# Kernel tuning notes

Hardware: AMD Instinct MI355X
Metric: run time of the kernel (lower is better)

## Reference

```python
import jax, jax.numpy as jnp
import numpy as np

B, T, L = 8, 5, 16          # meta-batch, inner (train) steps, test examples per task
C, H, W = 3, 64, 64
NCLS = 100
FEAT = 256 * (H // 16) * (W // 16)  # 4096
CHANS = [(C, 32), (32, 64), (64, 128), (128, 256), (256, 256)]
DN = ('NCHW', 'OIHW', 'NCHW')


def setup_inputs() -> dict:
    key = jax.random.key(0)
    ks = jax.random.split(key, 16)
    inp = {}
    for j, (ic, oc) in enumerate(CHANS):
        std = 1.0 / np.sqrt(ic * 9)
        inp[f"w{j}"] = jax.random.normal(ks[j], (oc, ic, 3, 3), jnp.float32) * std
        inp[f"b{j}"] = jnp.zeros((oc,), jnp.float32)
    inp["W_out"] = jax.random.normal(ks[5], (NCLS, FEAT), jnp.float32) / np.sqrt(FEAT)
    inp["b_out"] = jnp.zeros((NCLS,), jnp.float32)
    inp["inner_log_lr"] = jnp.asarray(np.log(0.01), jnp.float32)
    inp["train_x"] = jax.random.normal(ks[6], (B, T, C, H, W), jnp.float32)
    inp["test_x"] = jax.random.normal(ks[7], (B, L, C, H, W), jnp.float32)
    inp["train_gate"] = jax.random.uniform(ks[8], (B, T, FEAT), dtype=jnp.float32)
    inp["test_gate"] = jax.random.uniform(ks[9], (B, L, FEAT), dtype=jnp.float32)
    inp["train_y"] = jax.random.randint(ks[10], (B, T), 0, NCLS)
    inp["test_y"] = jax.random.randint(ks[11], (B, L), 0, NCLS)
    inp["evaluate"] = 1
    return inp


def _conv(x, w, b, s):
    # x: [N, C, H, W]; per-example weight w: [OC, IC, 3, 3]; 'same'-ish pad=1
    y = jax.lax.conv_general_dilated(x, w, (s, s), [(1, 1), (1, 1)], dimension_numbers=DN)
    return jax.nn.relu(y + b[None, :, None, None])


def _features(fw, x, gate):
    # x: [B, L, C, H, W]; fw: tuple of per-example (batched) params
    for j in range(5):
        s = 1 if j == 0 else 2
        x = jax.vmap(_conv, in_axes=(0, 0, 0, None))(x, fw[2 * j], fw[2 * j + 1], s)
    return x.reshape(x.shape[0], x.shape[1], -1) * gate  # [B, L, FEAT]


def _ce(logits, y):
    return -jnp.take_along_axis(jax.nn.log_softmax(logits, -1), y[..., None], -1)[..., 0]


def _forward(params, log_lr, train_x, test_x, train_gate, test_gate, train_y, test_y):
    b = train_x.shape[0]
    lr = jnp.exp(log_lr)
    # per-example fast weights (MAML)
    fw = tuple(jnp.broadcast_to(p, (b,) + p.shape) for p in params)

    def step(fw, batch):
        xi, yi, gi = batch  # [B,C,H,W], [B], [B,FEAT]
        def loss_fn(fw):
            f = _features(fw, xi[:, None], gi[:, None])[:, 0]  # [B, FEAT]
            logit = jnp.einsum('bnm,bm->bn', fw[10], f) + fw[11]
            return _ce(logit, yi).sum()
        g = jax.grad(loss_fn)(fw)
        return tuple(w - lr * gw for w, gw in zip(fw, g)), None

    fw, _ = jax.lax.scan(
        step, fw,
        (jnp.swapaxes(train_x, 0, 1), jnp.swapaxes(train_y, 0, 1), jnp.swapaxes(train_gate, 0, 1)))

    f = _features(fw, test_x, test_gate)                         # [B, L, FEAT]
    logit = jnp.einsum('bnm,blm->bln', fw[10], f) + fw[11][:, None, :]
    loss = _ce(logit, test_y)[..., None]                          # [B, L, 1]
    return loss, lr, logit


def reference(w0, b0, w1, b1, w2, b2, w3, b3, w4, b4, W_out, b_out, inner_log_lr,
              train_x, test_x, train_gate, test_gate, train_y, test_y, evaluate):
    params = (w0, b0, w1, b1, w2, b2, w3, b3, w4, b4, W_out, b_out)
    loss, lr, logit = _forward(params, inner_log_lr, train_x, test_x,
                               train_gate, test_gate, train_y, test_y)
    evaluation = (jnp.argmax(logit, -1) == test_y) if evaluate else None
    return (loss, lr, evaluation, logit)
```

## Files before the change

### kernel.cpp

```cpp
#include <hip/hip_runtime.h>

#define NB 8
#define NT 5
#define NL 16
#define NCLS 100
#define FEAT 4096
#define CHW (3*64*64)

#define OFF_W0 0
#define OFF_B0 864
#define OFF_W1 896
#define OFF_B1 19328
#define OFF_W2 19392
#define OFF_B2 93120
#define OFF_W3 93248
#define OFF_B3 388160
#define OFF_W4 388416
#define OFF_B4 978240
#define OFF_WO 978496
#define OFF_BO 1388096
#define PT     1388196

#define A1 0
#define A2 131072
#define A3 196608
#define A4 229376
#define A5 245760
#define ATOT 249856

struct Params12 { const float* p[12]; };

__global__ void bcast_kernel(Params12 ps, float* __restrict__ fw) {
    const int offs[13] = {OFF_W0,OFF_B0,OFF_W1,OFF_B1,OFF_W2,OFF_B2,OFF_W3,OFF_B3,
                          OFF_W4,OFF_B4,OFF_WO,OFF_BO,PT};
    long idx = (long)blockIdx.x * blockDim.x + threadIdx.x;
    long total = (long)NB * PT;
    if (idx >= total) return;
    int i = (int)(idx % PT);
    int j = 11;
    while (j > 0 && i < offs[j]) --j;
    fw[idx] = ps.p[j][i - offs[j]];
}

template<int IC,int IH,int IW,int OC,int OH,int OW,int S,int UF,int BS>
__global__ __launch_bounds__(BS) void conv_fwd_u(
    const float* __restrict__ xb, long x_ts,
    const float* __restrict__ fw, int woff, int boff,
    float* __restrict__ yb, long y_ts)
{
    constexpr int OHW = OH*OW, IHW = IH*IW;
    long idx = (long)blockIdx.x * BS + threadIdx.x;
    int pix = (int)(idx % OHW); long r = idx / OHW;
    int oc = (int)(r % OC); int b = (int)(r / OC);
    int oh = pix / OW, ow = pix % OW;
    int ih0 = oh*S - 1, iw0 = ow*S - 1;

    const float* x = xb + (long)b * x_ts;
    const float* w = fw + (long)b * PT + woff + (long)oc * IC * 9;
    float acc = fw[(long)b * PT + boff + oc];

    #pragma unroll 1
    for (int ic0 = 0; ic0 < IC; ic0 += UF) {
        float xv[UF][9];
        #pragma unroll
        for (int u = 0; u < UF; ++u) {
            const float* xc = x + (long)(ic0 + u) * IHW;
            #pragma unroll
            for (int kh = 0; kh < 3; ++kh) {
                int ih = ih0 + kh;
                #pragma unroll
                for (int kw = 0; kw < 3; ++kw) {
                    int iw = iw0 + kw;
                    bool v = ((unsigned)ih < (unsigned)IH) && ((unsigned)iw < (unsigned)IW);
                    xv[u][kh*3+kw] = v ? xc[ih*IW + iw] : 0.f;
                }
            }
        }
        #pragma unroll
        for (int u = 0; u < UF; ++u) {
            const float* wc = w + (ic0 + u) * 9;
            #pragma unroll
            for (int k = 0; k < 9; ++k)
                acc += xv[u][k] * wc[k];
        }
    }
    yb[(long)b * y_ts + (long)oc * OHW + pix] = fmaxf(acc, 0.f);
}

template<int IC,int IH,int IW,int OC,int OH,int OW,int S,int UF,int BS,int KS>
__global__ __launch_bounds__(BS) void conv_fwd_uks(
    const float* __restrict__ xb, long x_ts,
    const float* __restrict__ fw, int woff,
    float* __restrict__ pb)
{
    constexpr int OHW = OH*OW, IHW = IH*IW;
    constexpr int ICC = IC/KS;
    long idx = (long)blockIdx.x * BS + threadIdx.x;
    int pix = (int)(idx % OHW); long r = idx / OHW;
    int oc = (int)(r % OC); r /= OC;
    int ks = (int)(r % KS); int b = (int)(r / KS);
    int oh = pix / OW, ow = pix % OW;
    int ih0 = oh*S - 1, iw0 = ow*S - 1;

    const float* x = xb + (long)b * x_ts;
    const float* w = fw + (long)b * PT + woff + (long)oc * IC * 9;
    float acc = 0.f;

    #pragma unroll 1
    for (int ic0 = ks*ICC; ic0 < (ks+1)*ICC; ic0 += UF) {
        float xv[UF][9];
        #pragma unroll
        for (int u = 0; u < UF; ++u) {
            const float* xc = x + (long)(ic0 + u) * IHW;
            #pragma unroll
            for (int kh = 0; kh < 3; ++kh) {
                int ih = ih0 + kh;
                #pragma unroll
                for (int kw = 0; kw < 3; ++kw) {
                    int iw = iw0 + kw;
                    bool v = ((unsigned)ih < (unsigned)IH) && ((unsigned)iw < (unsigned)IW);
                    xv[u][kh*3+kw] = v ? xc[ih*IW + iw] : 0.f;
                }
            }
        }
        #pragma unroll
        for (int u = 0; u < UF; ++u) {
            const float* wc = w + (ic0 + u) * 9;
            #pragma unroll
            for (int k = 0; k < 9; ++k)
                acc += xv[u][k] * wc[k];
        }
    }
    pb[((long)ks*NB + b) * ((long)OC*OHW) + (long)oc*OHW + pix] = acc;
}

template<int IC,int IH,int IW,int OC,int OH,int OW,int S,int UF,int KS>
__global__ __launch_bounds__(64) void conv_fwd_us(
    const float* __restrict__ xb, long x_ts,
    const float* __restrict__ fw, int woff,
    float* __restrict__ pb)
{
    constexpr int OHW = OH*OW, IHW = IH*IW, ICC = IC/KS;
    static_assert(OHW == 64, "one wave = one oc-plane");
    int bi = blockIdx.x;
    int oc = bi % OC; int ks = (bi / OC) % KS; int b = bi / (OC*KS);
    int pix = threadIdx.x;
    int oh = pix / OW, ow = pix % OW;
    int ih0 = oh*S - 1, iw0 = ow*S - 1;

    const float* x = xb + (long)b * x_ts;
    const float* w = fw + (long)b * PT + woff + (long)oc * IC * 9;

    float acc = 0.f;
    #pragma unroll 1
    for (int ic0 = ks*ICC; ic0 < (ks+1)*ICC; ic0 += UF) {
        float xv[UF][9];
        #pragma unroll
        for (int u = 0; u < UF; ++u) {
            const float* xc = x + (long)(ic0 + u) * IHW;
            #pragma unroll
            for (int kh = 0; kh < 3; ++kh) {
                int ih = ih0 + kh;
                #pragma unroll
                for (int kw = 0; kw < 3; ++kw) {
                    int iw = iw0 + kw;
                    bool v = ((unsigned)ih < (unsigned)IH) && ((unsigned)iw < (unsigned)IW);
                    xv[u][kh*3+kw] = v ? xc[ih*IW + iw] : 0.f;
                }
            }
        }
        #pragma unroll
        for (int u = 0; u < UF; ++u) {
            const float* wc = w + (ic0 + u) * 9;
            #pragma unroll
            for (int k = 0; k < 9; ++k)
                acc += xv[u][k] * wc[k];
        }
    }
    pb[((long)ks*NB + b) * ((long)OC*OHW) + (long)oc*OHW + pix] = acc;
}

template<int IC,int IH,int IW,int OC,int OH,int OW,int S,int TOC,int NSUB,int ICB>
__global__ __launch_bounds__(256) void conv_fwd2(
    const float* __restrict__ xb, long x_ts, long x_es,
    const float* __restrict__ fw, int woff, int boff,
    float* __restrict__ yb, long y_ts, int N)
{
    constexpr int OHW = OH*OW, IHW = IH*IW;
    constexpr int PPB = 256/NSUB;
    constexpr int TILES = OHW/PPB;
    constexpr int OCB = NSUB*TOC;
    constexpr int NOCG = OC/OCB;
    __shared__ float wlds[ICB*9*OCB];

    int bi = blockIdx.x;
    int tile = bi % TILES;
    int ocg  = (bi / TILES) % NOCG;
    int n    = (bi / (TILES*NOCG)) % N;
    int b    = bi / (TILES*NOCG*N);

    int tid = threadIdx.x;
    int pixl = tid % PPB, sub = tid / PPB;
    int pix = tile * PPB + pixl;
    int oc0 = ocg * OCB + sub * TOC;
    int oh = pix / OW, ow = pix % OW;
    int ih0 = oh*S - 1, iw0 = ow*S - 1;

    const float* xp  = xb + (long)b * x_ts + (long)n * x_es;
    const float* fwp = fw + (long)b * PT + woff;
    const float* bp  = fw + (long)b * PT + boff;

    float acc[TOC];
    #pragma unroll
    for (int t = 0; t < TOC; ++t) acc[t] = bp[oc0 + t];

    #pragma unroll 1
    for (int ic0i = 0; ic0i < IC; ic0i += ICB) {
        __syncthreads();
        for (int i = tid; i < ICB*9*OCB; i += 256) {
            int o = i % OCB; int rem = i / OCB; int k = rem % 9; int icb = rem / 9;
            wlds[i] = fwp[((long)(ocg*OCB + o) * IC + ic0i + icb) * 9 + k];
        }
        __syncthreads();
        #pragma unroll 2
        for (int icb = 0; icb < ICB; ++icb) {
            const float* xc = xp + (long)(ic0i + icb) * IHW;
            float xv[9];
            #pragma unroll
            for (int kh = 0; kh < 3; ++kh)
            #pragma unroll
            for (int kw = 0; kw < 3; ++kw) {
                int ih = ih0 + kh, iw = iw0 + kw;
                bool v = ((unsigned)ih < (unsigned)IH) && ((unsigned)iw < (unsigned)IW);
                xv[kh*3+kw] = v ? xc[ih*IW + iw] : 0.f;
            }
            const float* wl = wlds + icb*9*OCB + sub*TOC;
            #pragma unroll
            for (int k = 0; k < 9; ++k) {
                #pragma unroll
                for (int t = 0; t < TOC; ++t)
                    acc[t] += xv[k] * wl[k*OCB + t];
            }
        }
    }

    float* yp = yb + (long)b * y_ts;
    #pragma unroll
    for (int t = 0; t < TOC; ++t)
        yp[((long)n*OC + oc0 + t) * OHW + pix] = fmaxf(acc[t], 0.f);
}

template<int IC,int IH,int IW,int OC,int OH,int OW,int S,int TOC,int NTOT,int KS>
__global__ __launch_bounds__(256) void conv_fwd2s(
    const float* __restrict__ xb, long x_ts, long x_es,
    const float* __restrict__ fw, int woff,
    float* __restrict__ pb)
{
    constexpr int OHW = OH*OW, IHW = IH*IW;
    constexpr int PSP = NTOT*OHW;
    constexpr int TILES = PSP/256;
    constexpr int NOCG = OC/TOC;
    constexpr int ICC = IC/KS;

    int bi = blockIdx.x;
    int tile = bi % TILES;
    int ocg  = (bi / TILES) % NOCG;
    int ks   = (bi / (TILES*NOCG)) % KS;
    int b    = bi / (TILES*NOCG*KS);

    int tid = threadIdx.x;
    int pixg = tile * 256 + tid;
    int n = pixg / OHW, pix = pixg % OHW;
    int oc0 = ocg * TOC;
    int oh = pix / OW, ow = pix % OW;
    int ih0 = oh*S - 1, iw0 = ow*S - 1;

    const float* xp = xb + (long)b * x_ts + (long)n * x_es;
    const float* wp = fw + (long)b * PT + woff;

    float acc[TOC];
    #pragma unroll
    for (int t = 0; t < TOC; ++t) acc[t] = 0.f;

    #pragma unroll 2
    for (int ic = ks*ICC; ic < (ks+1)*ICC; ++ic) {
        const float* xc = xp + (long)ic * IHW;
        float xv[9];
        #pragma unroll
        for (int kh = 0; kh < 3; ++kh)
        #pragma unroll
        for (int kw = 0; kw < 3; ++kw) {
            int ih = ih0 + kh, iw = iw0 + kw;
            bool v = ((unsigned)ih < (unsigned)IH) && ((unsigned)iw < (unsigned)IW);
            xv[kh*3+kw] = v ? xc[ih*IW + iw] : 0.f;
        }
        const float* wrow = wp + ((long)oc0 * IC + ic) * 9;
        #pragma unroll
        for (int t = 0; t < TOC; ++t) {
            const float* wt = wrow + (long)t * IC * 9;
            #pragma unroll
            for (int k = 0; k < 9; ++k)
                acc[t] += xv[k] * wt[k];
        }
    }

    float* yp = pb + ((long)ks * NB + b) * ((long)NTOT * OC * OHW);
    #pragma unroll
    for (int t = 0; t < TOC; ++t)
        yp[((long)n*OC + oc0 + t) * OHW + pix] = acc[t];
}

template<int KS>
__global__ __launch_bounds__(256) void ksum_relu(
    const float* __restrict__ pb, const float* __restrict__ fw, int boff,
    float* __restrict__ yb, long y_ts, int N, int OC, int OHW)
{
    long plane = (long)N * OC * OHW;
    long idx = (long)blockIdx.x * 256 + threadIdx.x;
    long total = (long)NB * plane;
    if (idx >= total) return;
    int b = (int)(idx / plane);
    long rem = idx % plane;
    int oc = (int)((rem / OHW) % OC);
    float s = fw[(long)b * PT + boff + oc];
    #pragma unroll
    for (int ks = 0; ks < KS; ++ks)
        s += pb[((long)ks * NB + b) * plane + rem];
    yb[(long)b * y_ts + rem] = fmaxf(s, 0.f);
}

template<int IC,int IH,int IW,int OC,int OH,int OW,int S,int OCT,int ICT,int OCPT,int OHC>
__global__ __launch_bounds__(256) void conv_bwd_dwg(
    float* __restrict__ fw, int woff, int boff,
    const float* __restrict__ dzbuf, int dz_off,
    const float* __restrict__ xb, long x_ts,
    const float* __restrict__ loglr)
{
    constexpr int OHW = OH*OW, IHW = IH*IW;
    constexpr int IW2 = IW + 2;
    constexpr int RW  = OHC*S + 1;
    constexpr int XPRAW = RW * IW2;
    constexpr int XP = XPRAW | 1;
    constexpr int OHWC = OHC*OW;
    constexpr int DZP = OHWC + 1;
    constexpr int NCH = OH/OHC;
    constexpr int OCSL = OCT/OCPT;
    static_assert(OCSL*ICT == 256, "block must be 256 threads");
    static_assert((OW & (OW-1)) == 0, "OW power of two");
    constexpr int LOG_OW = (OW==4) ? 2 : ((OW==8) ? 3 : 4);
    constexpr int NOCG = OC/OCT, NICG = IC/ICT;

    __shared__ float dzs[OCT*DZP];
    __shared__ float xs[ICT*XP];

    int bi = blockIdx.x;
    int icg = bi % NICG;
    int ocg = (bi / NICG) % NOCG;
    int b   = bi / (NICG*NOCG);
    int oc0 = ocg*OCT, ic0 = icg*ICT;

    int tid = threadIdx.x;
    int ic_sub = tid % ICT;
    int oc_sub = tid / ICT;

    const float* dzp = dzbuf + (long)b*ATOT + dz_off + (long)oc0*OHW;
    const float* xp  = xb + (long)b*x_ts + (long)ic0*IHW;

    float acc[OCPT][9];
    float accb[OCPT];
    #pragma unroll
    for (int p = 0; p < OCPT; ++p) {
        accb[p] = 0.f;
        #pragma unroll
        for (int k = 0; k < 9; ++k) acc[p][k] = 0.f;
    }

    for (int c = 0; c < NCH; ++c) {
        if (c) __syncthreads();
        for (int i = tid; i < OCT*OHWC; i += 256) {
            int oc = i / OHWC, j = i % OHWC;
            dzs[oc*DZP + j] = dzp[(long)oc*OHW + c*OHWC + j];
        }
        for (int i = tid; i < ICT*XPRAW; i += 256) {
            int ic = i / XPRAW, j = i % XPRAW;
            int r = j / IW2, col = j % IW2;
            int ih = c*(OHC*S) - 1 + r;
            int iw = col - 1;
            float v = 0.f;
            if ((unsigned)ih < (unsigned)IH && (unsigned)iw < (unsigned)IW)
                v = xp[(long)ic*IHW + ih*IW + iw];
            xs[ic*XP + j] = v;
        }
        __syncthreads();

        const float* dzr = dzs + oc_sub*DZP;
        const float* xr0 = xs + ic_sub*XP;
        #pragma unroll 2
        for (int pos = 0; pos < OHWC; ++pos) {
            int ohl = pos >> LOG_OW;
            int ow  = pos & (OW-1);
            const float* xr = xr0 + (ohl*S)*IW2 + ow*S;
            float xv[9];
            #pragma unroll
            for (int kh = 0; kh < 3; ++kh)
                #pragma unroll
                for (int kw = 0; kw < 3; ++kw)
                    xv[kh*3+kw] = xr[kh*IW2 + kw];
            #pragma unroll
            for (int p = 0; p < OCPT; ++p) {
                float dzv = dzr[p*OCSL*DZP + pos];
                accb[p] += dzv;
                #pragma unroll
                for (int k = 0; k < 9; ++k) acc[p][k] += dzv * xv[k];
            }
        }
    }

    float lr = expf(loglr[0]);
    #pragma unroll
    for (int p = 0; p < OCPT; ++p) {
        int oc = oc0 + p*OCSL + oc_sub;
        float* wp = fw + (long)b*PT + woff + ((long)oc*IC + ic0 + ic_sub)*9;
        #pragma unroll
        for (int k = 0; k < 9; ++k) wp[k] -= lr * acc[p][k];
        if (ic_sub == 0 && icg == 0)
            fw[(long)b*PT + boff + oc] -= lr * accb[p];
    }
}

__global__ void head_fwd(const float* __restrict__ a5b, long a_ts, long a_es,
                         const float* __restrict__ gb, long g_ts, long g_es,
                         const float* __restrict__ fw,
                         float* __restrict__ ob, long o_ts, long o_es, int N)
{
    int wid = (int)(((long)blockIdx.x * blockDim.x + threadIdx.x) >> 6);
    int lane = threadIdx.x & 63;
    int total = NB * N * NCLS;
    if (wid >= total) return;
    int cls = wid % NCLS; int r = wid / NCLS;
    int n = r % N; int b = r / N;
    const float* a5 = a5b + (long)b * a_ts + (long)n * a_es;
    const float* g  = gb  + (long)b * g_ts + (long)n * g_es;
    const float* W  = fw + (long)b * PT + OFF_WO + (long)cls * FEAT;
    float acc = 0.f;
    for (int m = lane; m < FEAT; m += 64) acc += W[m] * a5[m] * g[m];
    for (int off = 32; off; off >>= 1) acc += __shfl_down(acc, off, 64);
    if (lane == 0)
        ob[(long)b * o_ts + (long)n * o_es + cls] = acc + fw[(long)b * PT + OFF_BO + cls];
}

__global__ void softmax_dlogit(const float* __restrict__ logi, const int* __restrict__ ty, int t,
                               float* __restrict__ dlog)
{
    __shared__ float red[128];
    int b = blockIdx.x, tid = threadIdx.x;
    const float* lo = logi + b * NCLS;
    float v = (tid < NCLS) ? lo[tid] : -1e30f;
    red[tid] = v; __syncthreads();
    for (int s2 = 64; s2; s2 >>= 1) { if (tid < s2) red[tid] = fmaxf(red[tid], red[tid + s2]); __syncthreads(); }
    float mx = red[0]; __syncthreads();
    float e = (tid < NCLS) ? expf(v - mx) : 0.f;
    red[tid] = e; __syncthreads();
    for (int s2 = 64; s2; s2 >>= 1) { if (tid < s2) red[tid] += red[tid + s2]; __syncthreads(); }
    float sum = red[0];
    if (tid < NCLS) {
        int y = ty[b * NT + t];
        dlog[b * NCLS + tid] = e / sum - (tid == y ? 1.f : 0.f);
    }
}

__global__ void head_bwd_dz5(const float* __restrict__ fw, const float* __restrict__ dlog,
                             const float* __restrict__ ain, const float* __restrict__ gb, long g_ts,
                             float* __restrict__ dz)
{
    int idx = blockIdx.x * blockDim.x + threadIdx.x;
    if (idx >= NB * FEAT) return;
    int m = idx % FEAT, b = idx / FEAT;
    const float* W = fw + (long)b * PT + OFF_WO;
    float df = 0.f;
    for (int c = 0; c < NCLS; ++c) df += W[(long)c * FEAT + m] * dlog[b * NCLS + c];
    float a = ain[(long)b * ATOT + A5 + m];
    dz[(long)b * ATOT + A5 + m] = (a > 0.f) ? df * gb[(long)b * g_ts + m] : 0.f;
}

__global__ void head_update(float* __restrict__ fw, const float* __restrict__ dlog,
                            const float* __restrict__ ain, const float* __restrict__ gb, long g_ts,
                            const float* __restrict__ loglr)
{
    long idx = (long)blockIdx.x * blockDim.x + threadIdx.x;
    long total = (long)NB * NCLS * FEAT;
    if (idx >= total) return;
    int m = (int)(idx % FEAT); long r = idx / FEAT;
    int c = (int)(r % NCLS); int b = (int)(r / NCLS);
    float lr = expf(loglr[0]);
    float f = ain[(long)b * ATOT + A5 + m] * gb[(long)b * g_ts + m];
    float dl = dlog[b * NCLS + c];
    fw[(long)b * PT + OFF_WO + (long)c * FEAT + m] -= lr * dl * f;
    if (m == 0) fw[(long)b * PT + OFF_BO + c] -= lr * dl;
}

template<int IC,int IH,int IW,int OC,int OH,int OW,int ICG,int BLK>
__global__ __launch_bounds__(BLK) void conv_bwd_dx2(
    const float* __restrict__ dzbuf, int dz_off,
    const float* __restrict__ fw, int woff,
    const float* __restrict__ ain, int ain_off,
    float* __restrict__ dzin, int dzin_off)
{
    constexpr int IHW = IH*IW, OHW = OH*OW, NICG = IC/ICG, PB = IHW/BLK;
    __shared__ float wlds[OC*9*ICG];
    int bi = blockIdx.x;
    int pb  = bi % PB;
    int icg = (bi / PB) % NICG;
    int b   = bi / (PB * NICG);
    int ic0 = icg * ICG;
    const float* fwp = fw + (long)b * PT + woff;
    for (int i = threadIdx.x; i < OC*9*ICG; i += BLK) {
        int g = i % ICG; int rem = i / ICG; int k = rem % 9; int oc = rem / 9;
        wlds[i] = fwp[((long)oc * IC + ic0 + g) * 9 + k];
    }
    __syncthreads();

    int pix = pb * BLK + threadIdx.x;
    int ih = pix / IW, iw = pix % IW;
    int kh0 = (ih + 1) & 1, kw0 = (iw + 1) & 1;
    int ohA = (ih + 1 - kh0) >> 1, owA = (iw + 1 - kw0) >> 1;
    float mhA = (ohA < OH) ? 1.f : 0.f;   float mhB = (kh0 == 0) ? 1.f : 0.f;
    float mwA = (owA < OW) ? 1.f : 0.f;   float mwB = (kw0 == 0) ? 1.f : 0.f;
    int ohB = ohA - 1, owB = owA - 1;
    int ohAc = (ohA < OH) ? ohA : 0;  int owAc = (owA < OW) ? owA : 0;
    int ohBc = (ohB >= 0) ? ohB : 0;  int owBc = (owB >= 0) ? owB : 0;

    int oAA = ohAc*OW + owAc; float mAA = mhA*mwA; int kAA = kh0*3 + kw0;
    int oAB = ohAc*OW + owBc; float mAB = mhA*mwB; int kAB = kh0*3 + kw0 + 2;
    int oBA = ohBc*OW + owAc; float mBA = mhB*mwA; int kBA = (kh0+2)*3 + kw0;
    int oBB = ohBc*OW + owBc; float mBB = mhB*mwB; int kBB = (kh0+2)*3 + kw0 + 2;

    const float* dzp = dzbuf + (long)b * ATOT + dz_off;
    float acc[ICG];
    #pragma unroll
    for (int g = 0; g < ICG; ++g) acc[g] = 0.f;

    for (int oc = 0; oc < OC; ++oc) {
        const float* dzo = dzp + oc * OHW;
        float dAA = dzo[oAA] * mAA;
        float dAB = dzo[oAB] * mAB;
        float dBA = dzo[oBA] * mBA;
        float dBB = dzo[oBB] * mBB;
        const float* w = wlds + oc * 9 * ICG;
        #pragma unroll
        for (int g = 0; g < ICG; ++g)
            acc[g] += dAA * w[kAA*ICG+g] + dAB * w[kAB*ICG+g]
                    + dBA * w[kBA*ICG+g] + dBB * w[kBB*ICG+g];
    }
    #pragma unroll
    for (int g = 0; g < ICG; ++g) {
        long p = (long)b * ATOT + (long)(ic0 + g) * IHW + pix;
        float a = ain[p + ain_off];
        dzin[p + dzin_off] = (a > 0.f) ? acc[g] : 0.f;
    }
}

template<int IC,int IH,int IW,int OC,int OH,int OW,int S>
__global__ __launch_bounds__(64) void conv_bwd_dw2(
    float* __restrict__ fw, int woff, int boff,
    const float* __restrict__ dzbuf, int dz_off,
    const float* __restrict__ xb, long x_ts,
    const float* __restrict__ loglr)
{
    constexpr int OHW = OH*OW;
    int bi = blockIdx.x;
    int ic = bi % IC; int oc = (bi / IC) % OC; int b = bi / (IC * OC);
    int lane = threadIdx.x;
    const float* dzp = dzbuf + (long)b * ATOT + dz_off + (long)oc * OHW;
    const float* xp  = xb + (long)b * x_ts + (long)ic * IH * IW;

    float acc[10];
    #pragma unroll
    for (int k = 0; k < 10; ++k) acc[k] = 0.f;

    for (int pos = lane; pos < OHW; pos += 64) {
        float dzv = dzp[pos];
        int oh = pos / OW, ow = pos % OW;
        int ihb = oh * S - 1, iwb = ow * S - 1;
        acc[9] += dzv;
        #pragma unroll
        for (int kh = 0; kh < 3; ++kh) {
            int ih = ihb + kh;
            bool hv = ((unsigned)ih < (unsigned)IH);
            #pragma unroll
            for (int kw = 0; kw < 3; ++kw) {
                int iw = iwb + kw;
                float xv = (hv && (unsigned)iw < (unsigned)IW) ? xp[ih * IW + iw] : 0.f;
                acc[kh*3+kw] += dzv * xv;
            }
        }
    }
    #pragma unroll
    for (int k = 0; k < 10; ++k)
        for (int off = 32; off; off >>= 1) acc[k] += __shfl_down(acc[k], off, 64);

    if (lane == 0) {
        float lr = expf(loglr[0]);
        float* wp = fw + (long)b * PT + woff + ((long)oc * IC + ic) * 9;
        #pragma unroll
        for (int k = 0; k < 9; ++k) wp[k] -= lr * acc[k];
        if (ic == 0) fw[(long)b * PT + boff + oc] -= lr * acc[9];
    }
}

template<int IC,int IH,int IW,int OC,int OH,int OW,int S,int NSP>
__global__ __launch_bounds__(64) void conv_bwd_dw2s(
    float* __restrict__ pbuf,
    const float* __restrict__ dzbuf, int dz_off,
    const float* __restrict__ xb, long x_ts)
{
    constexpr int OHW = OH*OW, CH = OHW/NSP;
    int bi = blockIdx.x;
    int sp = bi % NSP; int ic = (bi / NSP) % IC;
    int oc = (bi / (NSP*IC)) % OC; int b = bi / (NSP*IC*OC);
    int lane = threadIdx.x;
    const float* dzp = dzbuf + (long)b * ATOT + dz_off + (long)oc * OHW;
    const float* xp  = xb + (long)b * x_ts + (long)ic * IH * IW;

    float acc[10];
    #pragma unroll
    for (int k = 0; k < 10; ++k) acc[k] = 0.f;

    for (int pos = sp*CH + lane; pos < sp*CH + CH; pos += 64) {
        float dzv = dzp[pos];
        int oh = pos / OW, ow = pos % OW;
        int ihb = oh * S - 1, iwb = ow * S - 1;
        acc[9] += dzv;
        #pragma unroll
        for (int kh = 0; kh < 3; ++kh) {
            int ih = ihb + kh;
            bool hv = ((unsigned)ih < (unsigned)IH);
            #pragma unroll
            for (int kw = 0; kw < 3; ++kw) {
                int iw = iwb + kw;
                float xv = (hv && (unsigned)iw < (unsigned)IW) ? xp[ih * IW + iw] : 0.f;
                acc[kh*3+kw] += dzv * xv;
            }
        }
    }
    #pragma unroll
    for (int k = 0; k < 10; ++k)
        for (int off = 32; off; off >>= 1) acc[k] += __shfl_down(acc[k], off, 64);

    if (lane == 0) {
        float* pp = pbuf + ((((long)sp*NB + b)*OC + oc)*IC + ic)*10;
        #pragma unroll
        for (int k = 0; k < 10; ++k) pp[k] = acc[k];
    }
}

template<int NSP>
__global__ void dw_finalize(const float* __restrict__ pbuf, float* __restrict__ fw,
                            int woff, int boff, const float* __restrict__ loglr,
                            int OC, int IC)
{
    int idx = blockIdx.x * blockDim.x + threadIdx.x;
    int total = NB * OC * IC * 10;
    if (idx >= total) return;
    int k = idx % 10; int r = idx / 10;
    int ic = r % IC; r /= IC;
    int oc = r % OC; int b = r / OC;
    float s = 0.f;
    #pragma unroll
    for (int sp = 0; sp < NSP; ++sp)
        s += pbuf[((((long)sp*NB + b)*OC + oc)*IC + ic)*10 + k];
    float lr = expf(loglr[0]);
    if (k < 9)
        fw[(long)b*PT + woff + ((long)oc*IC + ic)*9 + k] -= lr * s;
    else if (ic == 0)
        fw[(long)b*PT + boff + oc] -= lr * s;
}

__global__ void final_loss_eval(const float* __restrict__ logit_base,
                                const int* __restrict__ test_y,
                                float* __restrict__ out, int l0, int Lc)
{
    int idx = blockIdx.x * blockDim.x + threadIdx.x;
    if (idx >= NB * Lc) return;
    int n = idx % Lc, b = idx / Lc;
    int l = l0 + n;
    const float* lo = logit_base + ((long)b * NL + l) * NCLS;
    float mx = -1e30f; int am = 0;
    for (int c = 0; c < NCLS; ++c) { float v = lo[c]; if (v > mx) { mx = v; am = c; } }
    float se = 0.f;
    for (int c = 0; c < NCLS; ++c) se += expf(lo[c] - mx);
    int y = test_y[b * NL + l];
    out[b * NL + l] = -(lo[y] - mx - logf(se));
    out[129 + b * NL + l] = (am == y) ? 1.f : 0.f;
}

__global__ void write_lr(const float* __restrict__ loglr, float* __restrict__ out)
{
    if (threadIdx.x == 0 && blockIdx.x == 0) out[128] = expf(loglr[0]);
}

extern "C" void kernel_launch(void* const* d_in, const int* in_sizes, int n_in,
                              void* d_out, int out_size, void* d_ws, size_t ws_size,
                              hipStream_t stream)
{
    const float* loglr      = (const float*)d_in[12];
    const float* train_x    = (const float*)d_in[13];
    const float* test_x     = (const float*)d_in[14];
    const float* train_gate = (const float*)d_in[15];
    const float* test_gate  = (const float*)d_in[16];
    const int*   train_y    = (const int*)d_in[17];
    const int*   test_y     = (const int*)d_in[18];
    float* out = (float*)d_out;

    const long base = (long)NB*PT + 2L*NB*ATOT + 2L*NB*NCLS;
    int LCr = 4;
    if (ws_size >= (size_t)(base + 16L*1572864) * 4) LCr = 16;
    else if (ws_size >= (size_t)(base + 8L*1572864) * 4) LCr = 8;

    float* ws   = (float*)d_ws;
    float* FWp  = ws;
    float* AINp = FWp  + (long)NB * PT;
    float* DZp  = AINp + (long)NB * ATOT;
    float* LOGIp= DZp  + (long)NB * ATOT;
    float* DLOGp= LOGIp + NB * NCLS;
    float* TAp  = DLOGp + NB * NCLS;
    float* TBp  = TAp + (long)NB * LCr * 131072;

    float* P3t = TAp;
    float* P4t = TAp + 262144;
    float* PW0 = TAp + 262144 + 131072;

    Params12 ps;
    for (int j = 0; j < 12; ++j) ps.p[j] = (const float*)d_in[j];
    {
        long tot = (long)NB * PT;
        bcast_kernel<<<(int)((tot + 255) / 256), 256, 0, stream>>>(ps, FWp);
    }

    for (int t = 0; t < NT; ++t) {
        conv_fwd_u<3,64,64,32,64,64,1,3,256><<<4096, 256, 0, stream>>>(
            train_x + (long)t * CHW, (long)NT * CHW, FWp, OFF_W0, OFF_B0, AINp + A1, (long)ATOT);
        conv_fwd_u<32,64,64,64,32,32,2,4,256><<<2048, 256, 0, stream>>>(
            AINp + A1, (long)ATOT, FWp, OFF_W1, OFF_B1, AINp + A2, (long)ATOT);
        conv_fwd_u<64,32,32,128,16,16,2,4,256><<<1024, 256, 0, stream>>>(
            AINp + A2, (long)ATOT, FWp, OFF_W2, OFF_B2, AINp + A3, (long)ATOT);
        conv_fwd_us<128,16,16,256,8,8,2,4, 2><<<NB*2*256, 64, 0, stream>>>(
            AINp + A3, (long)ATOT, FWp, OFF_W3, P3t);
        ksum_relu<2><<<(NB*256*64 + 255) / 256, 256, 0, stream>>>(
            P3t, FWp, OFF_B3, AINp + A4, (long)ATOT, 1, 256, 64);
        conv_fwd_uks<256,8,8,256,4,4,2,8,64, 4><<<2048, 64, 0, stream>>>(
            AINp + A4, (long)ATOT, FWp, OFF_W4, P4t);
        ksum_relu<4><<<(NB*256*16 + 255) / 256, 256, 0, stream>>>(
            P4t, FWp, OFF_B4, AINp + A5, (long)ATOT, 1, 256, 16);

        {
            long waves = (long)NB * NCLS;
            head_fwd<<<(int)((waves * 64 + 255) / 256), 256, 0, stream>>>(
                AINp + A5, (long)ATOT, 0,
                train_gate + (long)t * FEAT, (long)NT * FEAT, 0,
                FWp, LOGIp, (long)NCLS, 0, 1);
        }
        softmax_dlogit<<<NB, 128, 0, stream>>>(LOGIp, train_y, t, DLOGp);
        head_bwd_dz5<<<(NB * FEAT + 255) / 256, 256, 0, stream>>>(
            FWp, DLOGp, AINp, train_gate + (long)t * FEAT, (long)NT * FEAT, DZp);
        {
            long tot = (long)NB * NCLS * FEAT;
            head_update<<<(int)((tot + 255) / 256), 256, 0, stream>>>(
                FWp, DLOGp, AINp, train_gate + (long)t * FEAT, (long)NT * FEAT, loglr);
        }

        conv_bwd_dx2<256,8,8,256,4,4,2,64><<<8*128, 64, 0, stream>>>(
            DZp, A5, FWp, OFF_W4, AINp, A4, DZp, A4);
        conv_bwd_dwg<256,8,8,256,4,4,2, 64,8,2, 4><<<1024, 256, 0, stream>>>(
            FWp, OFF_W4, OFF_B4, DZp, A5, AINp + A4, (long)ATOT, loglr);

        conv_bwd_dx2<128,16,16,256,8,8,4,256><<<8*32, 256, 0, stream>>>(
            DZp, A4, FWp, OFF_W3, AINp, A3, DZp, A3);
        conv_bwd_dwg<128,16,16,256,8,8,2, 64,8,2, 8><<<512, 256, 0, stream>>>(
            FWp, OFF_W3, OFF_B3, DZp, A4, AINp + A3, (long)ATOT, loglr);

        conv_bwd_dx2<64,32,32,128,16,16,4,256><<<8*16*4, 256, 0, stream>>>(
            DZp, A3, FWp, OFF_W2, AINp, A2, DZp, A2);
        conv_bwd_dwg<64,32,32,128,16,16,2, 32,8,1, 4><<<256, 256, 0, stream>>>(
            FWp, OFF_W2, OFF_B2, DZp, A3, AINp + A2, (long)ATOT, loglr);

        conv_bwd_dx2<32,64,64,64,32,32,4,256><<<8*8*16, 256, 0, stream>>>(
            DZp, A2, FWp, OFF_W1, AINp, A1, DZp, A1);
        conv_bwd_dw2<32,64,64,64,32,32,2><<<8*64*32, 64, 0, stream>>>(
            FWp, OFF_W1, OFF_B1, DZp, A2, AINp + A1, (long)ATOT, loglr);
        conv_bwd_dw2s<3,64,64,32,64,64,1, 8><<<8*32*3*8, 64, 0, stream>>>(
            PW0, DZp, A1, train_x + (long)t * CHW, (long)NT * CHW);
        dw_finalize<8><<<(NB*32*3*10 + 255) / 256, 256, 0, stream>>>(
            PW0, FWp, OFF_W0, OFF_B0, loglr, 32, 3);
    }

    if (LCr == 16) {
        conv_fwd2<3,64,64,32,64,64,1, 32,1,3><<<NB*16*16, 256, 0, stream>>>(
            test_x, (long)NL * CHW, CHW,
            FWp, OFF_W0, OFF_B0, TAp, 16L * 131072, 16);
        conv_fwd2<32,64,64,64,32,32,2, 16,1,8><<<NB*16*16, 256, 0, stream>>>(
            TAp, 16L * 131072, 131072,
            FWp, OFF_W1, OFF_B1, TBp, 16L * 65536, 16);
        conv_fwd2<64,32,32,128,16,16,2, 16,1,8><<<NB*16*8, 256, 0, stream>>>(
            TBp, 16L * 65536, 65536,
            FWp, OFF_W2, OFF_B2, TAp, 16L * 32768, 16);

        {
            float* P3 = TAp + 4194304;
            conv_fwd2s<128,16,16,256,8,8,2, 16,16, 4><<<NB*4*16*4, 256, 0, stream>>>(
                TAp, 16L * 32768, 32768, FWp, OFF_W3, P3);
            ksum_relu<4><<<(int)(((long)NB*16*256*64 + 255) / 256), 256, 0, stream>>>(
                P3, FWp, OFF_B3, TBp, 16L * 16384, 16, 256, 64);
        }
        {
            float* P4 = TBp + 2097152;
            conv_fwd2s<256,8,8,256,4,4,2, 16,16, 8><<<NB*8*16, 256, 0, stream>>>(
                TBp, 16L * 16384, 16384, FWp, OFF_W4, P4);
            ksum_relu<8><<<(int)(((long)NB*16*256*16 + 255) / 256), 256, 0, stream>>>(
                P4, FWp, OFF_B4, TAp, 16L * 4096, 16, 256, 16);
        }
        {
            long waves = (long)NB * 16 * NCLS;
            head_fwd<<<(int)((waves * 64 + 255) / 256), 256, 0, stream>>>(
                TAp, 16L * FEAT, FEAT,
                test_gate, (long)NL * FEAT, FEAT,
                FWp, out + 257, (long)NL * NCLS, NCLS, 16);
        }
    } else {
        for (int c = 0; c < NL / LCr; ++c) {
            int l0 = c * LCr;
            conv_fwd2<3,64,64,32,64,64,1, 32,1,3><<<NB*LCr*16, 256, 0, stream>>>(
                test_x + (long)l0 * CHW, (long)NL * CHW, CHW,
                FWp, OFF_W0, OFF_B0, TAp, (long)LCr * 131072, LCr);
            conv_fwd2<32,64,64,64,32,32,2, 16,1,8><<<NB*LCr*16, 256, 0, stream>>>(
                TAp, (long)LCr * 131072, 131072,
                FWp, OFF_W1, OFF_B1, TBp, (long)LCr * 65536, LCr);
            conv_fwd2<64,32,32,128,16,16,2, 16,1,8><<<NB*LCr*8, 256, 0, stream>>>(
                TBp, (long)LCr * 65536, 65536,
                FWp, OFF_W2, OFF_B2, TAp, (long)LCr * 32768, LCr);
            conv_fwd2<128,16,16,256,8,8,2, 8,4,8><<<NB*LCr*8, 256, 0, stream>>>(
                TAp, (long)LCr * 32768, 32768,
                FWp, OFF_W3, OFF_B3, TBp, (long)LCr * 16384, LCr);
            conv_fwd2<256,8,8,256,4,4,2, 4,16,8><<<NB*LCr*4, 256, 0, stream>>>(
                TBp, (long)LCr * 16384, 16384,
                FWp, OFF_W4, OFF_B4, TAp, (long)LCr * 4096, LCr);
            {
                long waves = (long)NB * LCr * NCLS;
                head_fwd<<<(int)((waves * 64 + 255) / 256), 256, 0, stream>>>(
                    TAp, (long)LCr * FEAT, FEAT,
                    test_gate + (long)l0 * FEAT, (long)NL * FEAT, FEAT,
                    FWp, out + 257 + (long)l0 * NCLS, (long)NL * NCLS, NCLS, LCr);
            }
        }
    }
    final_loss_eval<<<(NB * NL + 255) / 256, 256, 0, stream>>>(
        out + 257, test_y, out, 0, NL);
    write_lr<<<1, 1, 0, stream>>>(loglr, out);
}
```

Before: 4.133 ms.

## Stage strided conv input tiles in LDS with wave-uniform output-channel groups

Replaces the strided test-path forward conv kernels with a new kernel that loads padded input row tiles into shared memory per input-channel chunk. Each wave handles 64 pixels and a wave-uniform group of 16 output channels, so weight reads become scalar broadcasts. Layers 1 and 2 also move from conv_fwd2 to this kernel, with bias and ReLU fused when there is no split-K. The aim is fewer redundant global input reads and cheaper weight loads, at the cost of extra barriers and LDS use.

```diff
diff --git a/kernel.cpp b/kernel.cpp
--- a/kernel.cpp
+++ b/kernel.cpp
@@ -250,64 +250,105 @@
         yp[((long)n*OC + oc0 + t) * OHW + pix] = fmaxf(acc[t], 0.f);
 }
 
-template<int IC,int IH,int IW,int OC,int OH,int OW,int S,int TOC,int NTOT,int KS>
-__global__ __launch_bounds__(256) void conv_fwd2s(
+template<int IC,int IH,int IW,int OC,int OH,int OW,int S,
+         int NG,int TH,int ICB,int KS,int NTOT>
+__global__ __launch_bounds__(256) void conv_fwd_gx(
     const float* __restrict__ xb, long x_ts, long x_es,
-    const float* __restrict__ fw, int woff,
+    const float* __restrict__ fw, int woff, int boff,
+    float* __restrict__ yb, long y_ts,
     float* __restrict__ pb)
 {
     constexpr int OHW = OH*OW, IHW = IH*IW;
-    constexpr int PSP = NTOT*OHW;
-    constexpr int TILES = PSP/256;
-    constexpr int NOCG = OC/TOC;
+    constexpr int TOC = 16, OCB2 = 4*TOC;
+    constexpr int NOCG = OC/OCB2;
+    constexpr int RT = OH/TH;
+    constexpr int NGRP = NTOT/NG;
     constexpr int ICC = IC/KS;
+    constexpr int PW = IW + 1;
+    constexpr int PROWS = (TH-1)*S + 3;
+    constexpr int XPR = PROWS*PW;
+    constexpr int XP = XPR | 1;
+    static_assert(NG*TH*OW == 64, "lanes must cover exactly 64 pixels");
+    static_assert(S == 2, "padding derivation assumes stride 2");
+    static_assert(ICC % ICB == 0, "chunking");
+
+    __shared__ float xs[NG*ICB*XP];
 
     int bi = blockIdx.x;
-    int tile = bi % TILES;
-    int ocg  = (bi / TILES) % NOCG;
-    int ks   = (bi / (TILES*NOCG)) % KS;
-    int b    = bi / (TILES*NOCG*KS);
+    int ocg = bi % NOCG;
+    int rt  = (bi / NOCG) % RT;
+    int ng  = (bi / (NOCG*RT)) % NGRP;
+    int ks  = (bi / (NOCG*RT*NGRP)) % KS;
+    int b   = bi / (NOCG*RT*NGRP*KS);
 
     int tid = threadIdx.x;
-    int pixg = tile * 256 + tid;
-    int n = pixg / OHW, pix = pixg % OHW;
-    int oc0 = ocg * TOC;
-    int oh = pix / OW, ow = pix % OW;
-    int ih0 = oh*S - 1, iw0 = ow*S - 1;
-
-    const float* xp = xb + (long)b * x_ts + (long)n * x_es;
-    const float* wp = fw + (long)b * PT + woff;
+    int pl = tid & 63;
+    int ocsub = __builtin_amdgcn_readfirstlane(tid >> 6);
+    int nl = pl / (TH*OW);
+    int prow = (pl / OW) % TH;
+    int pcol = pl % OW;
+    int oc0 = ocg*OCB2 + ocsub*TOC;
+
+    const float* xbb = xb + (long)b * x_ts + (long)(ng*NG) * x_es;
+    const float* wb  = fw + (long)b * PT + woff;
 
     float acc[TOC];
     #pragma unroll
-    for (int t = 0; t < TOC; ++t) acc[t] = 0.f;
-
-    #pragma unroll 2
-    for (int ic = ks*ICC; ic < (ks+1)*ICC; ++ic) {
-        const float* xc = xp + (long)ic * IHW;
-        float xv[9];
-        #pragma unroll
-        for (int kh = 0; kh < 3; ++kh)
-        #pragma unroll
-        for (int kw = 0; kw < 3; ++kw) {
-            int ih = ih0 + kh, iw = iw0 + kw;
-            bool v = ((unsigned)ih < (unsigned)IH) && ((unsigned)iw < (unsigned)IW);
-            xv[kh*3+kw] = v ? xc[ih*IW + iw] : 0.f;
-        }
-        const float* wrow = wp + ((long)oc0 * IC + ic) * 9;
-        #pragma unroll
-        for (int t = 0; t < TOC; ++t) {
-            const float* wt = wrow + (long)t * IC * 9;
-            #pragma unroll
-            for (int k = 0; k < 9; ++k)
-                acc[t] += xv[k] * wt[k];
-        }
-    }
-
-    float* yp = pb + ((long)ks * NB + b) * ((long)NTOT * OC * OHW);
-    #pragma unroll
     for (int t = 0; t < TOC; ++t)
-        yp[((long)n*OC + oc0 + t) * OHW + pix] = acc[t];
+        acc[t] = (KS == 1) ? fw[(long)b*PT + boff + oc0 + t] : 0.f;
+
+    const int ih0t = rt*TH*S - 1;
+
+    #pragma unroll 1
+    for (int c = 0; c < ICC/ICB; ++c) {
+        int ic0 = ks*ICC + c*ICB;
+        if (c) __syncthreads();
+        for (int i = tid; i < NG*ICB*XPR; i += 256) {
+            int cc = i % PW;
+            int r  = (i / PW) % PROWS;
+            int icb = (i / (PW*PROWS)) % ICB;
+            int nl2 = i / (PW*PROWS*ICB);
+            int ih = ih0t + r, iw = cc - 1;
+            float v = 0.f;
+            if (ih >= 0 && iw >= 0)
+                v = xbb[(long)nl2 * x_es + (long)(ic0+icb)*IHW + ih*IW + iw];
+            xs[(nl2*ICB + icb)*XP + r*PW + cc] = v;
+        }
+        __syncthreads();
+        #pragma unroll 2
+        for (int icb = 0; icb < ICB; ++icb) {
+            int ic = ic0 + icb;
+            const float* xr = xs + (nl*ICB + icb)*XP + (prow*S)*PW + pcol*S;
+            float xv[9];
+            #pragma unroll
+            for (int kh = 0; kh < 3; ++kh)
+                #pragma unroll
+                for (int kw = 0; kw < 3; ++kw)
+                    xv[kh*3+kw] = xr[kh*PW + kw];
+            const float* wr = wb + ((long)oc0*IC + ic)*9;
+            #pragma unroll
+            for (int t = 0; t < TOC; ++t) {
+                const float* wt = wr + (long)t*IC*9;
+                #pragma unroll
+                for (int k = 0; k < 9; ++k)
+                    acc[t] += xv[k] * wt[k];
+            }
+        }
+    }
+
+    int n = ng*NG + nl;
+    int pix = (rt*TH + prow)*OW + pcol;
+    if (KS == 1) {
+        float* yp = yb + (long)b * y_ts;
+        #pragma unroll
+        for (int t = 0; t < TOC; ++t)
+            yp[((long)n*OC + oc0 + t)*OHW + pix] = fmaxf(acc[t], 0.f);
+    } else {
+        float* yp = pb + ((long)ks*NB + b) * ((long)NTOT*OC*OHW);
+        #pragma unroll
+        for (int t = 0; t < TOC; ++t)
+            yp[((long)n*OC + oc0 + t)*OHW + pix] = acc[t];
+    }
 }
 
 template<int KS>
@@ -798,24 +839,22 @@
         conv_fwd2<3,64,64,32,64,64,1, 32,1,3><<<NB*16*16, 256, 0, stream>>>(
             test_x, (long)NL * CHW, CHW,
             FWp, OFF_W0, OFF_B0, TAp, 16L * 131072, 16);
-        conv_fwd2<32,64,64,64,32,32,2, 16,1,8><<<NB*16*16, 256, 0, stream>>>(
-            TAp, 16L * 131072, 131072,
-            FWp, OFF_W1, OFF_B1, TBp, 16L * 65536, 16);
-        conv_fwd2<64,32,32,128,16,16,2, 16,1,8><<<NB*16*8, 256, 0, stream>>>(
-            TBp, 16L * 65536, 65536,
-            FWp, OFF_W2, OFF_B2, TAp, 16L * 32768, 16);
-
+
+        conv_fwd_gx<32,64,64, 64,32,32, 2, 1,2,8, 1, 16><<<2048, 256, 0, stream>>>(
+            TAp, 16L*131072, 131072, FWp, OFF_W1, OFF_B1, TBp, 16L*65536, nullptr);
+        conv_fwd_gx<64,32,32, 128,16,16, 2, 1,4,8, 1, 16><<<1024, 256, 0, stream>>>(
+            TBp, 16L*65536, 65536, FWp, OFF_W2, OFF_B2, TAp, 16L*32768, nullptr);
         {
             float* P3 = TAp + 4194304;
-            conv_fwd2s<128,16,16,256,8,8,2, 16,16, 4><<<NB*4*16*4, 256, 0, stream>>>(
-                TAp, 16L * 32768, 32768, FWp, OFF_W3, P3);
+            conv_fwd_gx<128,16,16, 256,8,8, 2, 1,8,8, 4, 16><<<2048, 256, 0, stream>>>(
+                TAp, 16L*32768, 32768, FWp, OFF_W3, 0, nullptr, 0, P3);
             ksum_relu<4><<<(int)(((long)NB*16*256*64 + 255) / 256), 256, 0, stream>>>(
                 P3, FWp, OFF_B3, TBp, 16L * 16384, 16, 256, 64);
         }
         {
             float* P4 = TBp + 2097152;
-            conv_fwd2s<256,8,8,256,4,4,2, 16,16, 8><<<NB*8*16, 256, 0, stream>>>(
-                TBp, 16L * 16384, 16384, FWp, OFF_W4, P4);
+            conv_fwd_gx<256,8,8, 256,4,4, 2, 4,4,8, 8, 16><<<1024, 256, 0, stream>>>(
+                TBp, 16L*16384, 16384, FWp, OFF_W4, 0, nullptr, 0, P4);
             ksum_relu<8><<<(int)(((long)NB*16*256*16 + 255) / 256), 256, 0, stream>>>(
                 P4, FWp, OFF_B4, TAp, 16L * 4096, 16, 256, 16);
         }
```

New measurement: 4.170 ms. Within noise of the previous version (+0.9%).
